# Performance work log

Measured on AMD Instinct MI355X. Metric: run time of the kernel, lower is better.

The kernel has to match this reference:

```python
import jax, jax.numpy as jnp
import numpy as np
from jax import lax

BS, SL, T = 1024, 512, 64


def setup_inputs() -> dict:
    key = jax.random.key(0)
    k_e, k_tags, k_st, k_et, k_t = jax.random.split(key, 5)
    e = jax.random.normal(k_e, (BS, SL, T), dtype=jnp.float32)
    tags = jax.random.randint(k_tags, (BS, SL), 0, T, dtype=jnp.int32)
    mask = jnp.ones((BS, SL), dtype=bool)
    st = jax.random.uniform(k_st, (T,), minval=-0.1, maxval=0.1, dtype=jnp.float32)
    et = jax.random.uniform(k_et, (T,), minval=-0.1, maxval=0.1, dtype=jnp.float32)
    t = jax.random.uniform(k_t, (T, T), minval=-0.1, maxval=0.1, dtype=jnp.float32)
    return {"e": e, "tags": tags, "mask": mask, "st": st, "et": et, "t": t}


def reference(e, tags, mask, st, et, t):
    # time-major: [sl, bs, T], [sl, bs], [sl, bs]
    e_t = jnp.transpose(e, (1, 0, 2))
    tags_t = tags.T
    mask_t = mask.T
    sl, bs = tags_t.shape
    idx = jnp.arange(bs)

    # gold path score and partition-function init at step 0
    score0 = st[tags_t[0]] + e_t[0, idx, tags_t[0]]          # [bs]
    norm0 = st[None, :] + e_t[0]                              # [bs, T]

    def step(carry, xs):
        score, normalize = carry
        tag_prev, tag_next, e_next, m_next = xs
        mf = m_next.astype(e_next.dtype)
        score = score + (t[tag_prev, tag_next] + e_next[idx, tag_next]) * mf
        # logsumexp over previous tag: [bs, T_prev, T_next] -> [bs, T_next]
        ns = jax.nn.logsumexp(normalize[:, :, None] + t[None, :, :] + e_next[:, None, :], axis=1)
        normalize = jnp.where(m_next[:, None], ns, normalize)
        return (score, normalize), None

    xs = (tags_t[:-1], tags_t[1:], e_t[1:], mask_t[1:])
    (score, normalize), _ = lax.scan(step, (score0, norm0), xs)

    last = mask_t.sum(axis=0) - 1                             # [bs]
    score = score + et[tags_t[last, idx]]
    logZ = jax.nn.logsumexp(normalize + et[None, :], axis=1)  # [bs]
    total = mask.sum().astype(e.dtype)
    return (score - logZ).sum() / total
```

## Files before the change

### kernel.cpp

```cpp
#include <hip/hip_runtime.h>
#include <hip/hip_bf16.h>

#define BS 1024
#define SL 512
#define T  64

typedef float f32x4 __attribute__((ext_vector_type(4)));
typedef short bf16x8 __attribute__((ext_vector_type(8)));
typedef int   i32x4  __attribute__((ext_vector_type(4)));

union FragU { i32x4 i; bf16x8 v; };

__device__ __forceinline__ float wave_reduce_sum(float x) {
#pragma unroll
    for (int m = 32; m >= 1; m >>= 1) x += __shfl_xor(x, m, 64);
    return x;
}

__device__ __forceinline__ int pk2(float a, float b) {
    union { __hip_bfloat162 h; int i; } u;
    u.h = __float22bfloat162_rn(make_float2(a, b));
    return u.i;
}

__device__ __forceinline__ float dpp_xor1(float x) {
    return __int_as_float(__builtin_amdgcn_update_dpp(
        0, __float_as_int(x), 0xB1, 0xF, 0xF, true));
}

#define MFMA16(A_, B_, C_) __builtin_amdgcn_mfma_f32_16x16x32_bf16((A_), (B_), (C_), 0, 0, 0)

#define BBUILD(BF_, C_, NT_)                                                  \
    {                                                                         \
        const int kb_ = q8 + 32 * (C_), nn_ = nbase + 16 * (NT_);             \
        FragU u_;                                                             \
        u_.i.x = pk2(__expf(t[(kb_ + 0) * sK + nn_ * sN]), __expf(t[(kb_ + 1) * sK + nn_ * sN])); \
        u_.i.y = pk2(__expf(t[(kb_ + 2) * sK + nn_ * sN]), __expf(t[(kb_ + 3) * sK + nn_ * sN])); \
        u_.i.z = pk2(__expf(t[(kb_ + 4) * sK + nn_ * sN]), __expf(t[(kb_ + 5) * sK + nn_ * sN])); \
        u_.i.w = pk2(__expf(t[(kb_ + 6) * sK + nn_ * sN]), __expf(t[(kb_ + 7) * sK + nn_ * sN])); \
        BF_ = u_.v;                                                           \
    }

#define STEP(EA_, EB_, APPLY_)                                                \
    {                                                                         \
        float geA_ = __expf(EA_);                                             \
        float geB_ = __expf(EB_);                                             \
        if (APPLY_) { geA_ *= pscale; geB_ *= pscale; }                       \
        f32x4 c0 = zf, c1 = zf, c2 = zf, c3 = zf;                             \
        c0 = MFMA16(A0, B00, c0); c1 = MFMA16(A0, B01, c1);                   \
        c2 = MFMA16(A0, B02, c2); c3 = MFMA16(A0, B03, c3);                   \
        c0 = MFMA16(A1, B10, c0); c1 = MFMA16(A1, B11, c1);                   \
        c2 = MFMA16(A1, B12, c2); c3 = MFMA16(A1, B13, c3);                   \
        const float sA_ = (g & 2) ? c1.x : c0.x;    \
        const float sB_ = (g & 2) ? c3.x : c2.x;    \
        sAc = sA_ * geA_;                                                     \
        sBc = sB_ * geB_;                                                     \
        const int pA_ = pk2(sAc, dpp_xor1(sAc));                              \
        const int pB_ = pk2(sBc, dpp_xor1(sBc));                              \
        FragU uA_, uB_;                                                       \
        uA_.i.x = __builtin_amdgcn_ds_bpermute(ad0, pA_);                     \
        uA_.i.y = __builtin_amdgcn_ds_bpermute(ad1, pA_);                     \
        uA_.i.z = __builtin_amdgcn_ds_bpermute(ad2, pA_);                     \
        uA_.i.w = __builtin_amdgcn_ds_bpermute(ad3, pA_);                     \
        uB_.i.x = __builtin_amdgcn_ds_bpermute(ad0, pB_);                     \
        uB_.i.y = __builtin_amdgcn_ds_bpermute(ad1, pB_);                     \
        uB_.i.z = __builtin_amdgcn_ds_bpermute(ad2, pB_);                     \
        uB_.i.w = __builtin_amdgcn_ds_bpermute(ad3, pB_);                     \
        A0 = uA_.v; A1 = uB_.v;                                               \
    }

#define RESCALE()                                                             \
    {                                                                         \
        const int mb_ = __builtin_amdgcn_readfirstlane(__float_as_int(sAc));  \
        const int ex_ = ((mb_ >> 23) & 0xff) - 126;                           \
        pscale = __int_as_float((127 - ex_) << 23);                           \
        logscale += (float)ex_ * 0.6931471805599453f;                         \
    }

#define EROW(Q_) (ebase + (size_t)(r0row + rdir * (Q_)) * T)

__global__ __launch_bounds__(128, 2)
void crf_fused_kernel(const float* __restrict__ e, const int* __restrict__ tags,
                      const float* __restrict__ st, const float* __restrict__ et,
                      const float* __restrict__ t, float* __restrict__ ws) {
    const int b = blockIdx.x;
    const int tid = threadIdx.x;
    const int w = tid >> 6;
    const int L = tid & 63;
    const int c = L & 15;
    const int g = L >> 4;
    const int q8 = g * 8;
    const int nbase = c;
    const float* ebase = e + (size_t)b * (SL * T);
    const int* tb = tags + b * SL;

    const int4 tg = *(const int4*)(tb + 4 * tid);
    const int tpv = (tid > 0) ? tb[4 * tid - 1] : 0;
    float scp;
    if (tid > 0) scp = t[(tpv << 6) + tg.x] + ebase[(size_t)(4 * tid) * T + tg.x];
    else         scp = st[tg.x] + ebase[tg.x];
    scp += t[(tg.x << 6) + tg.y] + ebase[(size_t)(4 * tid + 1) * T + tg.y];
    scp += t[(tg.y << 6) + tg.z] + ebase[(size_t)(4 * tid + 2) * T + tg.z];
    scp += t[(tg.z << 6) + tg.w] + ebase[(size_t)(4 * tid + 3) * T + tg.w];
    if (tid == 127) scp += et[tg.w];

    const int nA = c + 16 * (g >> 1);
    const int nB = nA + 32;

    const int adH = (g >> 1) << 7;
    const int ad0 = (((8 * g + 0) & 15) << 2) + adH;
    const int ad1 = (((8 * g + 2) & 15) << 2) + adH;
    const int ad2 = (((8 * g + 4) & 15) << 2) + adH;
    const int ad3 = (((8 * g + 6) & 15) << 2) + adH;

    const f32x4 zf = {0.f, 0.f, 0.f, 0.f};

    const int sK = w ? 1 : T;
    const int sN = w ? T : 1;
    const int r0row = w ? (SL - 1) : 0;
    const int rdir = w ? -1 : 1;

    bf16x8 B00, B01, B02, B03, B10, B11, B12, B13;
    BBUILD(B00, 0, 0) BBUILD(B01, 0, 1) BBUILD(B02, 0, 2) BBUILD(B03, 0, 3)
    BBUILD(B10, 1, 0) BBUILD(B11, 1, 1) BBUILD(B12, 1, 2) BBUILD(B13, 1, 3)

    bf16x8 A0, A1;
    {
        const float* er0 = ebase + (size_t)r0row * T;
        const float* bias = w ? et : st;
        const f32x4 ea0 = *(const f32x4*)(er0 + 8 * g);
        const f32x4 ea1 = *(const f32x4*)(er0 + 8 * g + 4);
        const f32x4 eb0 = *(const f32x4*)(er0 + 32 + 8 * g);
        const f32x4 eb1 = *(const f32x4*)(er0 + 32 + 8 * g + 4);
        const f32x4 s0 = *(const f32x4*)(bias + 8 * g);
        const f32x4 s1 = *(const f32x4*)(bias + 8 * g + 4);
        const f32x4 s2 = *(const f32x4*)(bias + 32 + 8 * g);
        const f32x4 s3 = *(const f32x4*)(bias + 32 + 8 * g + 4);
        FragU u0, u1;
        u0.i.x = pk2(__expf(ea0.x + s0.x), __expf(ea0.y + s0.y));
        u0.i.y = pk2(__expf(ea0.z + s0.z), __expf(ea0.w + s0.w));
        u0.i.z = pk2(__expf(ea1.x + s1.x), __expf(ea1.y + s1.y));
        u0.i.w = pk2(__expf(ea1.z + s1.z), __expf(ea1.w + s1.w));
        u1.i.x = pk2(__expf(eb0.x + s2.x), __expf(eb0.y + s2.y));
        u1.i.y = pk2(__expf(eb0.z + s2.z), __expf(eb0.w + s2.w));
        u1.i.z = pk2(__expf(eb1.x + s3.x), __expf(eb1.y + s3.y));
        u1.i.w = pk2(__expf(eb1.z + s3.z), __expf(eb1.w + s3.w));
        A0 = u0.v; A1 = u1.v;
    }

    float logscale = 0.0f;
    float pscale = 1.0f;
    float sAc = 0.0f, sBc = 0.0f;

    float rA0 = EROW(1)[nA], rA1 = EROW(2)[nA], rA2 = EROW(3)[nA], rA3 = EROW(4)[nA];
    float rA4 = EROW(5)[nA], rA5 = EROW(6)[nA], rA6 = EROW(7)[nA], rA7 = EROW(8)[nA];
    float rA8 = EROW(9)[nA], rA9 = EROW(10)[nA], rA10 = EROW(11)[nA], rA11 = EROW(12)[nA];
    float rB0 = EROW(1)[nB], rB1 = EROW(2)[nB], rB2 = EROW(3)[nB], rB3 = EROW(4)[nB];
    float rB4 = EROW(5)[nB], rB5 = EROW(6)[nB], rB6 = EROW(7)[nB], rB7 = EROW(8)[nB];
    float rB8 = EROW(9)[nB], rB9 = EROW(10)[nB], rB10 = EROW(11)[nB], rB11 = EROW(12)[nB];

    for (int base = 1; base <= 249; base += 4) {
        const int p0 = base + 12, p1 = base + 13, p2 = base + 14, p3 = base + 15;
        const float nA0 = EROW(p0)[nA], nA1 = EROW(p1)[nA];
        const float nA2 = EROW(p2)[nA], nA3 = EROW(p3)[nA];
        const float nB0 = EROW(p0)[nB], nB1 = EROW(p1)[nB];
        const float nB2 = EROW(p2)[nB], nB3 = EROW(p3)[nB];

        STEP(rA0, rB0, 1)
        STEP(rA1, rB1, 0)
        STEP(rA2, rB2, 0)
        STEP(rA3, rB3, 0)
        RESCALE()

        rA0 = rA4;  rA1 = rA5;  rA2 = rA6;  rA3 = rA7;
        rA4 = rA8;  rA5 = rA9;  rA6 = rA10; rA7 = rA11;
        rA8 = nA0;  rA9 = nA1;  rA10 = nA2; rA11 = nA3;
        rB0 = rB4;  rB1 = rB5;  rB2 = rB6;  rB3 = rB7;
        rB4 = rB8;  rB5 = rB9;  rB6 = rB10; rB7 = rB11;
        rB8 = nB0;  rB9 = nB1;  rB10 = nB2; rB11 = nB3;
    }
    if (w == 0) {
        STEP(rA0, rB0, 1)
        STEP(rA1, rB1, 0)
        STEP(rA2, rB2, 0)
        STEP(rA3, rB3, 0)
    } else {
        STEP(rA0, rB0, 1)
        STEP(rA1, rB1, 0)
        STEP(0.0f, 0.0f, 0)
    }

    __shared__ float fb2[2][T];
    __shared__ float lsW[2], scW[2];
    fb2[w][nA] = sAc;
    fb2[w][nB] = sBc;
    const float scs = wave_reduce_sum(scp);
    if (L == 0) { lsW[w] = logscale; scW[w] = scs; }
    __syncthreads();
    if (w == 0) {
        float zz = fb2[0][L] * fb2[1][L];
        zz = wave_reduce_sum(zz);
        if (L == 0)
            ws[b] = (scW[0] + scW[1]) - (__logf(zz) + lsW[0] + lsW[1]);
    }
}

__global__ __launch_bounds__(256)
void final_kernel(const float* __restrict__ ws, float* __restrict__ out) {
    const int tid = threadIdx.x;
    float x = (ws[tid] + ws[tid + 256]) + (ws[tid + 512] + ws[tid + 768]);
    x = wave_reduce_sum(x);
    __shared__ float sm[4];
    if ((tid & 63) == 0) sm[tid >> 6] = x;
    __syncthreads();
    if (tid == 0) out[0] = ((sm[0] + sm[1]) + (sm[2] + sm[3])) / (float)(BS * SL);
}

extern "C" void kernel_launch(void* const* d_in, const int* in_sizes, int n_in,
                              void* d_out, int out_size, void* d_ws, size_t ws_size,
                              hipStream_t stream) {
    const float* e    = (const float*)d_in[0];
    const int*   tags = (const int*)d_in[1];
    const float* st   = (const float*)d_in[3];
    const float* et   = (const float*)d_in[4];
    const float* t    = (const float*)d_in[5];
    float* out = (float*)d_out;
    float* ws  = (float*)d_ws;

    crf_fused_kernel<<<BS, 128, 0, stream>>>(e, tags, st, et, t, ws);
    final_kernel<<<1, 256, 0, stream>>>(ws, out);
}
```

Baseline: 268.8 us.

## Swap MFMA operand roles and redistribute state with permlane swaps instead of bpermute

The transition matrix now serves as the MFMA A operand and the forward state as the broadcast B operand. The recurrence state is rebuilt into B fragments with permlane32/permlane16 swap instructions instead of eight ds_bpermute calls per step, which removes the LDS-path shuffles from the serial critical chain. Emission prefetch changes to vectorized f32x4 row loads with a rolling four-step register buffer. The cost is more VALU work per step: every lane does 16 exps and extra multiplies on the redundant broadcast columns, and register pressure is higher.

```diff
diff --git a/kernel.cpp b/kernel.cpp
--- a/kernel.cpp
+++ b/kernel.cpp
@@ -8,6 +8,7 @@
 typedef float f32x4 __attribute__((ext_vector_type(4)));
 typedef short bf16x8 __attribute__((ext_vector_type(8)));
 typedef int   i32x4  __attribute__((ext_vector_type(4)));
+typedef unsigned int u32x2 __attribute__((ext_vector_type(2)));
 
 union FragU { i32x4 i; bf16x8 v; };
 
@@ -23,61 +24,75 @@
     return u.i;
 }
 
-__device__ __forceinline__ float dpp_xor1(float x) {
-    return __int_as_float(__builtin_amdgcn_update_dpp(
-        0, __float_as_int(x), 0xB1, 0xF, 0xF, true));
-}
-
 #define MFMA16(A_, B_, C_) __builtin_amdgcn_mfma_f32_16x16x32_bf16((A_), (B_), (C_), 0, 0, 0)
 
-#define BBUILD(BF_, C_, NT_)                                                  \
-    {                                                                         \
-        const int kb_ = q8 + 32 * (C_), nn_ = nbase + 16 * (NT_);             \
+#define ABUILD(AF_, KT_, MT_)                                                 \
+    {                                                                         \
+        const int kb_ = q8 + 32 * (KT_), nn_ = c + 16 * (MT_);                \
         FragU u_;                                                             \
         u_.i.x = pk2(__expf(t[(kb_ + 0) * sK + nn_ * sN]), __expf(t[(kb_ + 1) * sK + nn_ * sN])); \
         u_.i.y = pk2(__expf(t[(kb_ + 2) * sK + nn_ * sN]), __expf(t[(kb_ + 3) * sK + nn_ * sN])); \
         u_.i.z = pk2(__expf(t[(kb_ + 4) * sK + nn_ * sN]), __expf(t[(kb_ + 5) * sK + nn_ * sN])); \
         u_.i.w = pk2(__expf(t[(kb_ + 6) * sK + nn_ * sN]), __expf(t[(kb_ + 7) * sK + nn_ * sN])); \
+        AF_ = u_.v;                                                           \
+    }
+
+#define REB(BF_, VA_, VB_)                                                    \
+    {                                                                         \
+        const u32x2 sx_ = __builtin_amdgcn_permlane32_swap(__float_as_uint(VA_.x), __float_as_uint(VB_.x), false, false); \
+        const u32x2 tx_ = __builtin_amdgcn_permlane16_swap(sx_.x, sx_.y, false, false); \
+        const u32x2 sy_ = __builtin_amdgcn_permlane32_swap(__float_as_uint(VA_.y), __float_as_uint(VB_.y), false, false); \
+        const u32x2 ty_ = __builtin_amdgcn_permlane16_swap(sy_.x, sy_.y, false, false); \
+        const u32x2 sz_ = __builtin_amdgcn_permlane32_swap(__float_as_uint(VA_.z), __float_as_uint(VB_.z), false, false); \
+        const u32x2 tz_ = __builtin_amdgcn_permlane16_swap(sz_.x, sz_.y, false, false); \
+        const u32x2 sw_ = __builtin_amdgcn_permlane32_swap(__float_as_uint(VA_.w), __float_as_uint(VB_.w), false, false); \
+        const u32x2 tw_ = __builtin_amdgcn_permlane16_swap(sw_.x, sw_.y, false, false); \
+        FragU u_;                                                             \
+        u_.i.x = pk2(__uint_as_float(tx_.x), __uint_as_float(ty_.x));         \
+        u_.i.y = pk2(__uint_as_float(tz_.x), __uint_as_float(tw_.x));         \
+        u_.i.z = pk2(__uint_as_float(tx_.y), __uint_as_float(ty_.y));         \
+        u_.i.w = pk2(__uint_as_float(tz_.y), __uint_as_float(tw_.y));         \
         BF_ = u_.v;                                                           \
     }
 
-#define STEP(EA_, EB_, APPLY_)                                                \
-    {                                                                         \
-        float geA_ = __expf(EA_);                                             \
-        float geB_ = __expf(EB_);                                             \
-        if (APPLY_) { geA_ *= pscale; geB_ *= pscale; }                       \
-        f32x4 c0 = zf, c1 = zf, c2 = zf, c3 = zf;                             \
-        c0 = MFMA16(A0, B00, c0); c1 = MFMA16(A0, B01, c1);                   \
-        c2 = MFMA16(A0, B02, c2); c3 = MFMA16(A0, B03, c3);                   \
-        c0 = MFMA16(A1, B10, c0); c1 = MFMA16(A1, B11, c1);                   \
-        c2 = MFMA16(A1, B12, c2); c3 = MFMA16(A1, B13, c3);                   \
-        const float sA_ = (g & 2) ? c1.x : c0.x;    \
-        const float sB_ = (g & 2) ? c3.x : c2.x;    \
-        sAc = sA_ * geA_;                                                     \
-        sBc = sB_ * geB_;                                                     \
-        const int pA_ = pk2(sAc, dpp_xor1(sAc));                              \
-        const int pB_ = pk2(sBc, dpp_xor1(sBc));                              \
-        FragU uA_, uB_;                                                       \
-        uA_.i.x = __builtin_amdgcn_ds_bpermute(ad0, pA_);                     \
-        uA_.i.y = __builtin_amdgcn_ds_bpermute(ad1, pA_);                     \
-        uA_.i.z = __builtin_amdgcn_ds_bpermute(ad2, pA_);                     \
-        uA_.i.w = __builtin_amdgcn_ds_bpermute(ad3, pA_);                     \
-        uB_.i.x = __builtin_amdgcn_ds_bpermute(ad0, pB_);                     \
-        uB_.i.y = __builtin_amdgcn_ds_bpermute(ad1, pB_);                     \
-        uB_.i.z = __builtin_amdgcn_ds_bpermute(ad2, pB_);                     \
-        uB_.i.w = __builtin_amdgcn_ds_bpermute(ad3, pB_);                     \
-        A0 = uA_.v; A1 = uB_.v;                                               \
+#define STEPN(Q0_, Q1_, Q2_, Q3_, APPLY_)                                     \
+    {                                                                         \
+        f32x4 g0_, g1_, g2_, g3_;                                             \
+        g0_.x = __expf(Q0_.x); g0_.y = __expf(Q0_.y);                         \
+        g0_.z = __expf(Q0_.z); g0_.w = __expf(Q0_.w);                         \
+        g1_.x = __expf(Q1_.x); g1_.y = __expf(Q1_.y);                         \
+        g1_.z = __expf(Q1_.z); g1_.w = __expf(Q1_.w);                         \
+        g2_.x = __expf(Q2_.x); g2_.y = __expf(Q2_.y);                         \
+        g2_.z = __expf(Q2_.z); g2_.w = __expf(Q2_.w);                         \
+        g3_.x = __expf(Q3_.x); g3_.y = __expf(Q3_.y);                         \
+        g3_.z = __expf(Q3_.z); g3_.w = __expf(Q3_.w);                         \
+        if (APPLY_) { g0_ *= pscale; g1_ *= pscale; g2_ *= pscale; g3_ *= pscale; } \
+        f32x4 d0_ = zf, d1_ = zf, d2_ = zf, d3_ = zf;                         \
+        d0_ = MFMA16(A00, B0, d0_); d1_ = MFMA16(A10, B0, d1_);               \
+        d2_ = MFMA16(A20, B0, d2_); d3_ = MFMA16(A30, B0, d3_);               \
+        d0_ = MFMA16(A01, B1, d0_); d1_ = MFMA16(A11, B1, d1_);               \
+        d2_ = MFMA16(A21, B1, d2_); d3_ = MFMA16(A31, B1, d3_);               \
+        v0 = d0_ * g0_; v1 = d1_ * g1_; v2 = d2_ * g2_; v3 = d3_ * g3_;      \
+        REB(B0, v0, v1)                                                       \
+        REB(B1, v2, v3)                                                       \
     }
 
 #define RESCALE()                                                             \
     {                                                                         \
-        const int mb_ = __builtin_amdgcn_readfirstlane(__float_as_int(sAc));  \
+        const int mb_ = __builtin_amdgcn_readfirstlane(__float_as_int(v0.x)); \
         const int ex_ = ((mb_ >> 23) & 0xff) - 126;                           \
         pscale = __int_as_float((127 - ex_) << 23);                           \
         logscale += (float)ex_ * 0.6931471805599453f;                         \
     }
 
-#define EROW(Q_) (ebase + (size_t)(r0row + rdir * (Q_)) * T)
+#define PREFN(Q0_, Q1_, Q2_, Q3_, S_)                                         \
+    {                                                                         \
+        const float* p_ = ebase + (size_t)(r0row + rdir * (S_)) * T + 4 * g;  \
+        Q0_ = *(const f32x4*)(p_);                                            \
+        Q1_ = *(const f32x4*)(p_ + 16);                                       \
+        Q2_ = *(const f32x4*)(p_ + 32);                                       \
+        Q3_ = *(const f32x4*)(p_ + 48);                                       \
+    }
 
 __global__ __launch_bounds__(128, 2)
 void crf_fused_kernel(const float* __restrict__ e, const int* __restrict__ tags,
@@ -90,7 +105,6 @@
     const int c = L & 15;
     const int g = L >> 4;
     const int q8 = g * 8;
-    const int nbase = c;
     const float* ebase = e + (size_t)b * (SL * T);
     const int* tb = tags + b * SL;
 
@@ -104,15 +118,6 @@
     scp += t[(tg.z << 6) + tg.w] + ebase[(size_t)(4 * tid + 3) * T + tg.w];
     if (tid == 127) scp += et[tg.w];
 
-    const int nA = c + 16 * (g >> 1);
-    const int nB = nA + 32;
-
-    const int adH = (g >> 1) << 7;
-    const int ad0 = (((8 * g + 0) & 15) << 2) + adH;
-    const int ad1 = (((8 * g + 2) & 15) << 2) + adH;
-    const int ad2 = (((8 * g + 4) & 15) << 2) + adH;
-    const int ad3 = (((8 * g + 6) & 15) << 2) + adH;
-
     const f32x4 zf = {0.f, 0.f, 0.f, 0.f};
 
     const int sK = w ? 1 : T;
@@ -120,11 +125,13 @@
     const int r0row = w ? (SL - 1) : 0;
     const int rdir = w ? -1 : 1;
 
-    bf16x8 B00, B01, B02, B03, B10, B11, B12, B13;
-    BBUILD(B00, 0, 0) BBUILD(B01, 0, 1) BBUILD(B02, 0, 2) BBUILD(B03, 0, 3)
-    BBUILD(B10, 1, 0) BBUILD(B11, 1, 1) BBUILD(B12, 1, 2) BBUILD(B13, 1, 3)
-
-    bf16x8 A0, A1;
+    bf16x8 A00, A01, A10, A11, A20, A21, A30, A31;
+    ABUILD(A00, 0, 0) ABUILD(A01, 1, 0)
+    ABUILD(A10, 0, 1) ABUILD(A11, 1, 1)
+    ABUILD(A20, 0, 2) ABUILD(A21, 1, 2)
+    ABUILD(A30, 0, 3) ABUILD(A31, 1, 3)
+
+    bf16x8 B0, B1;
     {
         const float* er0 = ebase + (size_t)r0row * T;
         const float* bias = w ? et : st;
@@ -145,55 +152,50 @@
         u1.i.y = pk2(__expf(eb0.z + s2.z), __expf(eb0.w + s2.w));
         u1.i.z = pk2(__expf(eb1.x + s3.x), __expf(eb1.y + s3.y));
         u1.i.w = pk2(__expf(eb1.z + s3.z), __expf(eb1.w + s3.w));
-        A0 = u0.v; A1 = u1.v;
+        B0 = u0.v; B1 = u1.v;
     }
 
     float logscale = 0.0f;
     float pscale = 1.0f;
-    float sAc = 0.0f, sBc = 0.0f;
-
-    float rA0 = EROW(1)[nA], rA1 = EROW(2)[nA], rA2 = EROW(3)[nA], rA3 = EROW(4)[nA];
-    float rA4 = EROW(5)[nA], rA5 = EROW(6)[nA], rA6 = EROW(7)[nA], rA7 = EROW(8)[nA];
-    float rA8 = EROW(9)[nA], rA9 = EROW(10)[nA], rA10 = EROW(11)[nA], rA11 = EROW(12)[nA];
-    float rB0 = EROW(1)[nB], rB1 = EROW(2)[nB], rB2 = EROW(3)[nB], rB3 = EROW(4)[nB];
-    float rB4 = EROW(5)[nB], rB5 = EROW(6)[nB], rB6 = EROW(7)[nB], rB7 = EROW(8)[nB];
-    float rB8 = EROW(9)[nB], rB9 = EROW(10)[nB], rB10 = EROW(11)[nB], rB11 = EROW(12)[nB];
+    f32x4 v0, v1, v2, v3;
+
+    f32x4 q00, q01, q02, q03, q10, q11, q12, q13;
+    f32x4 q20, q21, q22, q23, q30, q31, q32, q33;
+    PREFN(q00, q01, q02, q03, 1)
+    PREFN(q10, q11, q12, q13, 2)
+    PREFN(q20, q21, q22, q23, 3)
+    PREFN(q30, q31, q32, q33, 4)
 
     for (int base = 1; base <= 249; base += 4) {
-        const int p0 = base + 12, p1 = base + 13, p2 = base + 14, p3 = base + 15;
-        const float nA0 = EROW(p0)[nA], nA1 = EROW(p1)[nA];
-        const float nA2 = EROW(p2)[nA], nA3 = EROW(p3)[nA];
-        const float nB0 = EROW(p0)[nB], nB1 = EROW(p1)[nB];
-        const float nB2 = EROW(p2)[nB], nB3 = EROW(p3)[nB];
-
-        STEP(rA0, rB0, 1)
-        STEP(rA1, rB1, 0)
-        STEP(rA2, rB2, 0)
-        STEP(rA3, rB3, 0)
+        STEPN(q00, q01, q02, q03, 1)
+        PREFN(q00, q01, q02, q03, base + 4)
+        STEPN(q10, q11, q12, q13, 0)
+        PREFN(q10, q11, q12, q13, base + 5)
+        STEPN(q20, q21, q22, q23, 0)
+        PREFN(q20, q21, q22, q23, base + 6)
+        STEPN(q30, q31, q32, q33, 0)
         RESCALE()
-
-        rA0 = rA4;  rA1 = rA5;  rA2 = rA6;  rA3 = rA7;
-        rA4 = rA8;  rA5 = rA9;  rA6 = rA10; rA7 = rA11;
-        rA8 = nA0;  rA9 = nA1;  rA10 = nA2; rA11 = nA3;
-        rB0 = rB4;  rB1 = rB5;  rB2 = rB6;  rB3 = rB7;
-        rB4 = rB8;  rB5 = rB9;  rB6 = rB10; rB7 = rB11;
-        rB8 = nB0;  rB9 = nB1;  rB10 = nB2; rB11 = nB3;
+        PREFN(q30, q31, q32, q33, base + 7)
     }
     if (w == 0) {
-        STEP(rA0, rB0, 1)
-        STEP(rA1, rB1, 0)
-        STEP(rA2, rB2, 0)
-        STEP(rA3, rB3, 0)
+        STEPN(q00, q01, q02, q03, 1)
+        STEPN(q10, q11, q12, q13, 0)
+        STEPN(q20, q21, q22, q23, 0)
+        STEPN(q30, q31, q32, q33, 0)
     } else {
-        STEP(rA0, rB0, 1)
-        STEP(rA1, rB1, 0)
-        STEP(0.0f, 0.0f, 0)
-    }
-
-    __shared__ float fb2[2][T];
+        STEPN(q00, q01, q02, q03, 1)
+        STEPN(q10, q11, q12, q13, 0)
+        STEPN(zf, zf, zf, zf, 0)
+    }
+
+    __shared__ __attribute__((aligned(16))) float fb2[2][T];
     __shared__ float lsW[2], scW[2];
-    fb2[w][nA] = sAc;
-    fb2[w][nB] = sBc;
+    if (c == 0) {
+        *(f32x4*)&fb2[w][ 0 + 4 * g] = v0;
+        *(f32x4*)&fb2[w][16 + 4 * g] = v1;
+        *(f32x4*)&fb2[w][32 + 4 * g] = v2;
+        *(f32x4*)&fb2[w][48 + 4 * g] = v3;
+    }
     const float scs = wave_reduce_sum(scp);
     if (L == 0) { lsW[w] = logscale; scW[w] = scs; }
     __syncthreads();
```

Measured after the change: 335.0 us. 24.6% more time.
